# Kernel optimization log

Hardware: AMD Instinct MI355X
Metric: run time of the kernel (lower is better)

Reference implementation:

```python
import jax, jax.numpy as jnp
import numpy as np
import math

LOG2 = math.log(2)
B, N, H, E, M = 128, 2048, 300, 20, 200
IN = 3 * H + 3 * E  # 960: [mem, query, mem*query, 3 feature embs]
NEG = -10000.0


def _bucket(x):
    # floor(log2(x)) + 3 for x > 4, identity for x <= 4, clamped to [0, 9]
    xf = x.astype(jnp.float32)
    logspace = jnp.floor(jnp.log(jnp.maximum(xf, 1.0)) / LOG2).astype(jnp.int32) + 3
    return jnp.clip(jnp.where(x <= 4, x, logspace), 0, 9)


def setup_inputs() -> dict:
    key = jax.random.key(0)
    ks = jax.random.split(key, 12)
    return {
        "query_vector": jax.random.normal(ks[0], (B, H), jnp.float32),
        "ment_score": jax.random.normal(ks[1], (B,), jnp.float32),
        "mem_vectors": jax.random.normal(ks[2], (B, N, H), jnp.float32),
        "ent_counter": jax.random.randint(ks[3], (B, N), 0, 20, jnp.int32),
        "distances": jax.random.randint(ks[4], (B, N), 0, 5000, jnp.int32),
        "last_action_idx": jax.random.randint(ks[5], (B,), 0, 5, jnp.int32),
        "cell_idx": jax.random.randint(ks[6], (B,), 0, N, jnp.int32),
        "W1": jax.random.normal(ks[7], (IN, M), jnp.float32) / np.sqrt(IN),
        "b1": jnp.zeros((M,), jnp.float32),
        "W2": jax.random.normal(ks[8], (M, 1), jnp.float32) / np.sqrt(M),
        "b2": jnp.zeros((1,), jnp.float32),
        "dist_table": jax.random.normal(ks[9], (10, E), jnp.float32),
        "count_table": jax.random.normal(ks[10], (10, E), jnp.float32),
        "action_table": jax.random.normal(ks[11], (5, E), jnp.float32),
    }


def reference(query_vector, ment_score, mem_vectors, ent_counter, distances,
              last_action_idx, cell_idx, W1, b1, W2, b2,
              dist_table, count_table, action_table):
    # ---- feature embeddings (get_feature_embs, litbank: dist+counter+last_action) ----
    dist_emb = dist_table[_bucket(distances)]            # [B, N, E]
    cnt_emb = count_table[_bucket(ent_counter)]          # [B, N, E]
    act_emb = jnp.broadcast_to(action_table[last_action_idx][:, None, :], (B, N, E))
    feature_embs = jnp.concatenate([dist_emb, cnt_emb, act_emb], axis=-1)  # [B, N, 3E]

    # ---- get_coref_new_scores ----
    q = jnp.broadcast_to(query_vector[:, None, :], (B, N, H))
    pair_vec = jnp.concatenate([mem_vectors, q, mem_vectors * q, feature_embs], axis=-1)  # [B, N, IN]
    hdn = jax.nn.relu(jnp.einsum('bni,im->bnm', pair_vec, W1) + b1)
    pair_score = (jnp.einsum('bnm,mo->bno', hdn, W2) + b2)[..., 0]  # [B, N]
    coref_score = pair_score + ment_score[:, None]

    mask = (ent_counter > 0).astype(jnp.float32)                            # [B, N]
    full_mask = jnp.concatenate([mask, jnp.ones((B, 1), jnp.float32)], axis=1)
    full_score = jnp.concatenate([coref_score, jnp.zeros((B, 1), jnp.float32)], axis=1)
    coref_new_scores = full_score * full_mask + (1.0 - full_mask) * NEG     # [B, N+1]

    # ---- coref_update (entity_rep='max' default branch: running average + masked scatter) ----
    brange = jnp.arange(B)
    cnt_sel = ent_counter[brange, cell_idx].astype(jnp.float32)             # [B]
    mem_sel = mem_vectors[brange, cell_idx]                                 # [B, H]
    avg_vec = (mem_sel * cnt_sel[:, None] + query_vector) / (cnt_sel[:, None] + 1.0)
    onehot = (jnp.arange(N)[None, :] == cell_idx[:, None]).astype(jnp.float32)[:, :, None]  # [B, N, 1]
    new_mem = mem_vectors * (1.0 - onehot) + onehot * avg_vec[:, None, :]

    return coref_new_scores, new_mem
```

## Files before the change

### kernel.cpp

```cpp
#include <hip/hip_runtime.h>
#include <math.h>

#define BB 128
#define NN 2048
#define HH 300
#define EE 20
#define MM 200
#define NEGV (-10000.0f)
#define SCORES_OFF (BB * (NN + 1))

#define NCOL 208
#define KSTEPS 10
#define ROWSH 72
#define KIMG (NCOL * ROWSH)
#define BIMG_SHORTS ((size_t)BB * KSTEPS * KIMG)
#define FWS_FLOATS (BB * MM + 10 * MM + 10 * MM + BB * HH)

typedef short bf16x8 __attribute__((ext_vector_type(8)));
typedef float f32x4 __attribute__((ext_vector_type(4)));

__device__ __forceinline__ int bucketf(int x) {
  if (x <= 4) return x < 0 ? 0 : x;
  float l = floorf(logf((float)x) / 0.69314718055994530942f);
  int bi = (int)l + 3;
  return bi > 9 ? 9 : bi;
}

__device__ __forceinline__ short f2bf(float f) {
  union { float f; unsigned u; } v; v.f = f;
  unsigned r = (v.u + 0x7FFFu + ((v.u >> 16) & 1u)) >> 16;
  return (short)r;
}
__device__ __forceinline__ float bf2f(short s) {
  union { unsigned u; float f; } v; v.u = ((unsigned)(unsigned short)s) << 16;
  return v.f;
}

__global__ void k_small(const float* __restrict__ W1, const float* __restrict__ b1,
                        const float* __restrict__ q, const float* __restrict__ mem,
                        const float* __restrict__ dtab, const float* __restrict__ ctab,
                        const float* __restrict__ atab, const int* __restrict__ lact,
                        const int* __restrict__ entc, const int* __restrict__ cell,
                        float* __restrict__ distW, float* __restrict__ cntW,
                        float* __restrict__ bias, float* __restrict__ avg,
                        float* __restrict__ out) {
  const int blk = blockIdx.x;
  const int tid = threadIdx.x;
  if (blk < 13) {
    int idx = blk * 320 + tid;
    if (idx >= 2 * 10 * MM) return;
    int t = idx / (10 * MM);
    int r = idx % (10 * MM);
    int d = r / MM;
    int m = r % MM;
    const float* tab = (t == 0) ? dtab : ctab;
    int wrow0 = (t == 0) ? (3 * HH) : (3 * HH + EE);
    float s = 0.f;
#pragma unroll
    for (int e = 0; e < EE; e++) s += tab[d * EE + e] * W1[(wrow0 + e) * MM + m];
    ((t == 0) ? distW : cntW)[d * MM + m] = s;
  } else if (blk < 93) {
    int idx = (blk - 13) * 320 + tid;
    if (idx >= BB * MM) return;
    int b = idx / MM;
    int m = idx % MM;
    float s = b1[m];
    for (int h = 0; h < HH; h++) s += q[b * HH + h] * W1[(HH + h) * MM + m];
    int la = lact[b];
#pragma unroll
    for (int e = 0; e < EE; e++)
      s += atab[la * EE + e] * W1[(3 * HH + 2 * EE + e) * MM + m];
    bias[idx] = s;
  } else {
    int b = blk - 93;
    int ci = cell[b];
    if (tid < HH) {
      float c = (float)entc[b * NN + ci];
      float m = mem[((size_t)b * NN + ci) * HH + tid];
      avg[b * HH + tid] = (m * c + q[b * HH + tid]) / (c + 1.f);
    } else if (tid == HH) {
      out[b * (NN + 1) + NN] = 0.f;
    }
  }
}

__global__ void k_prep(const float* __restrict__ W1, const float* __restrict__ q,
                       short* __restrict__ Bimg) {
  int idx = blockIdx.x * blockDim.x + threadIdx.x;
  if (idx >= BB * KSTEPS * NCOL) return;
  int col = idx % NCOL;
  int bks = idx / NCOL;
  int ks = bks % KSTEPS;
  int b = bks / KSTEPS;
  int k0 = ks * 32;
  const float* qb = q + b * HH;

  __align__(16) short buf[ROWSH];
#pragma unroll
  for (int g = 0; g < 4; g++) {
#pragma unroll
    for (int i = 0; i < 8; i++) {
      int k = k0 + 8 * g + i;
      float val = 0.f;
      if (k < HH && col < MM) {
        val = fmaf(qb[k], W1[(size_t)(2 * HH + k) * MM + col],
                   W1[(size_t)k * MM + col]);
      }
      short h = f2bf(val);
      buf[g * 8 + i] = h;
      buf[32 + g * 8 + i] = f2bf(val - bf2f(h));
    }
  }
#pragma unroll
  for (int i = 64; i < 72; i++) buf[i] = 0;

  float4* dst = (float4*)(Bimg + (size_t)idx * ROWSH);
  const float4* src = (const float4*)buf;
#pragma unroll
  for (int i = 0; i < 9; i++) dst[i] = src[i];
}

__device__ __forceinline__ void epilogue(
    const f32x4* acc, int b, int n0, int w, int lr, int g,
    const float* __restrict__ bias, const float* __restrict__ distW,
    const float* __restrict__ cntW, const float* __restrict__ W2,
    const float* __restrict__ b2, const float* __restrict__ ment,
    const int* __restrict__ entc, const int* __restrict__ dist,
    float* __restrict__ out) {
  const float addc = b2[0] + ment[b];
  const float* bi = bias + b * MM;
  float s[4];
#pragma unroll
  for (int r = 0; r < 4; r++) {
    int nr = n0 + w * 16 + 4 * g + r;
    int db = bucketf(dist[b * NN + nr]);
    int cb = bucketf(entc[b * NN + nr]);
    const float* dW = distW + db * MM;
    const float* cW = cntW + cb * MM;
    float acc_s = 0.f;
#pragma unroll
    for (int f = 0; f < 13; f++) {
      if (f < 12 || lr < 8) {
        int m = f * 16 + lr;
        float h = acc[f][r] + bi[m] + dW[m] + cW[m];
        acc_s += fmaxf(h, 0.f) * W2[m];
      }
    }
    s[r] = acc_s;
  }
#pragma unroll
  for (int off = 1; off < 16; off <<= 1) {
#pragma unroll
    for (int r = 0; r < 4; r++) s[r] += __shfl_xor(s[r], off);
  }
  if (lr == 0) {
#pragma unroll
    for (int r = 0; r < 4; r++) {
      int nr = n0 + w * 16 + 4 * g + r;
      int mk = entc[b * NN + nr] > 0;
      out[b * (NN + 1) + nr] = mk ? (s[r] + addc) : NEGV;
    }
  }
}

__device__ __forceinline__ void load_a(
    const float* rowp, float* orow, const float* avgp, bool subst, int kb,
    bf16x8* ahi, bf16x8* alo) {
  float va[8];
  if (kb + 7 < HH) {
    float4 x0 = *(const float4*)(rowp + kb);
    float4 x1 = *(const float4*)(rowp + kb + 4);
    va[0] = x0.x; va[1] = x0.y; va[2] = x0.z; va[3] = x0.w;
    va[4] = x1.x; va[5] = x1.y; va[6] = x1.z; va[7] = x1.w;
    float4 o0 = x0, o1 = x1;
    if (subst) {
      o0 = *(const float4*)(avgp + kb);
      o1 = *(const float4*)(avgp + kb + 4);
    }
    *(float4*)(orow + kb) = o0;
    *(float4*)(orow + kb + 4) = o1;
  } else {
#pragma unroll
    for (int i = 0; i < 8; i++) {
      int k = kb + i;
      bool ok = (k < HH);
      va[i] = ok ? rowp[k] : 0.f;
      if (ok) orow[k] = subst ? avgp[k] : va[i];
    }
  }
#pragma unroll
  for (int i = 0; i < 8; i++) {
    short h = f2bf(va[i]);
    (*ahi)[i] = h;
    (*alo)[i] = f2bf(va[i] - bf2f(h));
  }
}

__global__ __launch_bounds__(256, 3) void k_main(
    const float* __restrict__ mem, const short* __restrict__ Bimg,
    const float* __restrict__ bias, const float* __restrict__ distW,
    const float* __restrict__ cntW, const float* __restrict__ W2,
    const float* __restrict__ b2, const float* __restrict__ ment,
    const int* __restrict__ entc, const int* __restrict__ dist,
    const int* __restrict__ cell, const float* __restrict__ avg,
    float* __restrict__ out) {
  __shared__ __align__(16) short btS[KIMG];

  const int tid = threadIdx.x;
  const int bid = blockIdx.x;
  const int b = (bid & 7) * 16 + (bid >> 8);
  const int n0 = ((bid >> 3) & 31) * 64;

  const int w = tid >> 6;
  const int l = tid & 63;
  const int lr = l & 15;
  const int g = l >> 4;

  const int ci = cell[b];
  const int n = n0 + w * 16 + lr;
  const float* rowp = mem + ((size_t)b * NN + n) * HH;
  float* orow = out + SCORES_OFF + ((size_t)b * NN + n) * HH;
  const float* avgp = avg + b * HH;
  const bool subst = (n == ci);

  f32x4 acc[13];
#pragma unroll
  for (int f = 0; f < 13; f++) acc[f] = (f32x4){0.f, 0.f, 0.f, 0.f};

  for (int ks = 0; ks < KSTEPS; ks++) {
    bf16x8 ahi, alo;
    load_a(rowp, orow, avgp, subst, ks * 32 + 8 * g, &ahi, &alo);

    __syncthreads();
    {
      const float4* bsrc = (const float4*)(Bimg + (size_t)(b * KSTEPS + ks) * KIMG);
      float4* bdst = (float4*)btS;
      for (int i = tid; i < KIMG / 8; i += 256) bdst[i] = bsrc[i];
    }
    __syncthreads();

#pragma unroll
    for (int f = 0; f < 13; f++) {
      const short* bp = &btS[(f * 16 + lr) * ROWSH + g * 8];
      bf16x8 bhi = *(const bf16x8*)bp;
      bf16x8 blo = *(const bf16x8*)(bp + 32);
      acc[f] = __builtin_amdgcn_mfma_f32_16x16x32_bf16(ahi, bhi, acc[f], 0, 0, 0);
      acc[f] = __builtin_amdgcn_mfma_f32_16x16x32_bf16(alo, bhi, acc[f], 0, 0, 0);
      acc[f] = __builtin_amdgcn_mfma_f32_16x16x32_bf16(ahi, blo, acc[f], 0, 0, 0);
    }
  }

  epilogue(acc, b, n0, w, lr, g, bias, distW, cntW, W2, b2, ment, entc, dist, out);
}

__global__ __launch_bounds__(256, 3) void k_main_fb(
    const float* __restrict__ mem, const float* __restrict__ W1,
    const float* __restrict__ q, const float* __restrict__ bias,
    const float* __restrict__ distW, const float* __restrict__ cntW,
    const float* __restrict__ W2, const float* __restrict__ b2,
    const float* __restrict__ ment, const int* __restrict__ entc,
    const int* __restrict__ dist, const int* __restrict__ cell,
    const float* __restrict__ avg, float* __restrict__ out) {
  __shared__ __align__(16) short btS[KIMG];

  const int tid = threadIdx.x;
  const int b = blockIdx.y;
  const int n0 = blockIdx.x * 64;
  const int w = tid >> 6;
  const int l = tid & 63;
  const int lr = l & 15;
  const int g = l >> 4;

  const int ci = cell[b];
  const int n = n0 + w * 16 + lr;
  const float* rowp = mem + ((size_t)b * NN + n) * HH;
  float* orow = out + SCORES_OFF + ((size_t)b * NN + n) * HH;
  const float* avgp = avg + b * HH;
  const bool subst = (n == ci);
  const float* qb = q + b * HH;

  f32x4 acc[13];
#pragma unroll
  for (int f = 0; f < 13; f++) acc[f] = (f32x4){0.f, 0.f, 0.f, 0.f};

  for (int ks = 0; ks < KSTEPS; ks++) {
    const int k0 = ks * 32;
    bf16x8 ahi, alo;
    load_a(rowp, orow, avgp, subst, k0 + 8 * g, &ahi, &alo);

    __syncthreads();
    for (int it = 0; it < 4; it++) {
      int idx = tid + it * 256;
      if (idx < 832) {
        int col = idx % NCOL;
        int gg = idx / NCOL;
        int kbb = k0 + 8 * gg;
        bf16x8 h8, l8;
#pragma unroll
        for (int i = 0; i < 8; i++) {
          int k = kbb + i;
          float val = 0.f;
          if (k < HH && col < MM) {
            val = fmaf(qb[k], W1[(size_t)(2 * HH + k) * MM + col],
                       W1[(size_t)k * MM + col]);
          }
          short h = f2bf(val);
          h8[i] = h;
          l8[i] = f2bf(val - bf2f(h));
        }
        short* dst = &btS[col * ROWSH + gg * 8];
        *(bf16x8*)dst = h8;
        *(bf16x8*)(dst + 32) = l8;
      }
    }
    __syncthreads();

#pragma unroll
    for (int f = 0; f < 13; f++) {
      const short* bp = &btS[(f * 16 + lr) * ROWSH + g * 8];
      bf16x8 bhi = *(const bf16x8*)bp;
      bf16x8 blo = *(const bf16x8*)(bp + 32);
      acc[f] = __builtin_amdgcn_mfma_f32_16x16x32_bf16(ahi, bhi, acc[f], 0, 0, 0);
      acc[f] = __builtin_amdgcn_mfma_f32_16x16x32_bf16(alo, bhi, acc[f], 0, 0, 0);
      acc[f] = __builtin_amdgcn_mfma_f32_16x16x32_bf16(ahi, blo, acc[f], 0, 0, 0);
    }
  }

  epilogue(acc, b, n0, w, lr, g, bias, distW, cntW, W2, b2, ment, entc, dist, out);
}

extern "C" void kernel_launch(void* const* d_in, const int* in_sizes, int n_in,
                              void* d_out, int out_size, void* d_ws, size_t ws_size,
                              hipStream_t stream) {
  const float* q    = (const float*)d_in[0];
  const float* ment = (const float*)d_in[1];
  const float* mem  = (const float*)d_in[2];
  const int* entc   = (const int*)d_in[3];
  const int* dist   = (const int*)d_in[4];
  const int* lact   = (const int*)d_in[5];
  const int* cell   = (const int*)d_in[6];
  const float* W1   = (const float*)d_in[7];
  const float* b1   = (const float*)d_in[8];
  const float* W2   = (const float*)d_in[9];
  const float* b2   = (const float*)d_in[10];
  const float* dtab = (const float*)d_in[11];
  const float* ctab = (const float*)d_in[12];
  const float* atab = (const float*)d_in[13];
  float* out = (float*)d_out;

  const size_t need_fast = BIMG_SHORTS * sizeof(short) + FWS_FLOATS * sizeof(float);
  const bool fast = (ws_size >= need_fast);

  short* Bimg = (short*)d_ws;
  float* fws  = fast ? (float*)(Bimg + BIMG_SHORTS) : (float*)d_ws;
  float* bias  = fws;
  float* distW = bias + BB * MM;
  float* cntW  = distW + 10 * MM;
  float* avg   = cntW + 10 * MM;

  k_small<<<221, 320, 0, stream>>>(W1, b1, q, mem, dtab, ctab, atab, lact,
                                   entc, cell, distW, cntW, bias, avg, out);
  if (fast) {
    k_prep<<<(BB * KSTEPS * NCOL) / 256, 256, 0, stream>>>(W1, q, Bimg);
    k_main<<<4096, 256, 0, stream>>>(mem, Bimg, bias, distW, cntW, W2, b2,
                                     ment, entc, dist, cell, avg, out);
  } else {
    k_main_fb<<<dim3(NN / 64, BB), 256, 0, stream>>>(
        mem, W1, q, bias, distW, cntW, W2, b2, ment, entc, dist, cell, avg, out);
  }
}
```

Before: 775.0 us.

## Double-buffer B tiles via global_load_lds and prefetch A rows in main GEMM

Measured after the change: 708.3 us. -8.6%, faster.

```diff
diff --git a/kernel.cpp b/kernel.cpp
--- a/kernel.cpp
+++ b/kernel.cpp
@@ -13,8 +13,8 @@
 #define KSTEPS 10
 #define ROWSH 72
 #define KIMG (NCOL * ROWSH)
+#define CH16 (KIMG / 8)
 #define BIMG_SHORTS ((size_t)BB * KSTEPS * KIMG)
-#define FWS_FLOATS (BB * MM + 10 * MM + 10 * MM + BB * HH)
 
 typedef short bf16x8 __attribute__((ext_vector_type(8)));
 typedef float f32x4 __attribute__((ext_vector_type(4)));
@@ -36,14 +36,20 @@
   return v.f;
 }
 
-__global__ void k_small(const float* __restrict__ W1, const float* __restrict__ b1,
+__device__ __forceinline__ void gload16(const void* g, void* l) {
+  __builtin_amdgcn_global_load_lds(
+      (const __attribute__((address_space(1))) void*)g,
+      (__attribute__((address_space(3))) void*)l, 16, 0, 0);
+}
+
+__global__ void k_prep2(const float* __restrict__ W1, const float* __restrict__ b1,
                         const float* __restrict__ q, const float* __restrict__ mem,
                         const float* __restrict__ dtab, const float* __restrict__ ctab,
                         const float* __restrict__ atab, const int* __restrict__ lact,
                         const int* __restrict__ entc, const int* __restrict__ cell,
                         float* __restrict__ distW, float* __restrict__ cntW,
                         float* __restrict__ bias, float* __restrict__ avg,
-                        float* __restrict__ out) {
+                        short* __restrict__ Bimg, float* __restrict__ out) {
   const int blk = blockIdx.x;
   const int tid = threadIdx.x;
   if (blk < 13) {
@@ -71,7 +77,7 @@
     for (int e = 0; e < EE; e++)
       s += atab[la * EE + e] * W1[(3 * HH + 2 * EE + e) * MM + m];
     bias[idx] = s;
-  } else {
+  } else if (blk < 221) {
     int b = blk - 93;
     int ci = cell[b];
     if (tid < HH) {
@@ -81,43 +87,81 @@
     } else if (tid == HH) {
       out[b * (NN + 1) + NN] = 0.f;
     }
-  }
-}
-
-__global__ void k_prep(const float* __restrict__ W1, const float* __restrict__ q,
-                       short* __restrict__ Bimg) {
-  int idx = blockIdx.x * blockDim.x + threadIdx.x;
-  if (idx >= BB * KSTEPS * NCOL) return;
-  int col = idx % NCOL;
-  int bks = idx / NCOL;
-  int ks = bks % KSTEPS;
-  int b = bks / KSTEPS;
-  int k0 = ks * 32;
-  const float* qb = q + b * HH;
-
-  __align__(16) short buf[ROWSH];
-#pragma unroll
-  for (int g = 0; g < 4; g++) {
+  } else {
+    int idx = (blk - 221) * 320 + tid;
+    int col = idx % NCOL;
+    int bks = idx / NCOL;
+    int ks = bks % KSTEPS;
+    int b = bks / KSTEPS;
+    int k0 = ks * 32;
+    const float* qb = q + b * HH;
+    short* dst = Bimg + (size_t)idx * ROWSH;
+#pragma unroll
+    for (int g = 0; g < 4; g++) {
+      bf16x8 h8, l8;
+#pragma unroll
+      for (int i = 0; i < 8; i++) {
+        int k = k0 + 8 * g + i;
+        float val = 0.f;
+        if (k < HH && col < MM) {
+          val = fmaf(qb[k], W1[(size_t)(2 * HH + k) * MM + col],
+                     W1[(size_t)k * MM + col]);
+        }
+        short h = f2bf(val);
+        h8[i] = h;
+        l8[i] = f2bf(val - bf2f(h));
+      }
+      *(bf16x8*)(dst + g * 8) = h8;
+      *(bf16x8*)(dst + 32 + g * 8) = l8;
+    }
+    *(bf16x8*)(dst + 64) = (bf16x8){0, 0, 0, 0, 0, 0, 0, 0};
+  }
+}
+
+__device__ __forceinline__ void issueA(const float* rowp, int kb, float* va) {
+  if (kb + 7 < HH) {
+    float4 x0 = *(const float4*)(rowp + kb);
+    float4 x1 = *(const float4*)(rowp + kb + 4);
+    va[0] = x0.x; va[1] = x0.y; va[2] = x0.z; va[3] = x0.w;
+    va[4] = x1.x; va[5] = x1.y; va[6] = x1.z; va[7] = x1.w;
+  } else {
 #pragma unroll
     for (int i = 0; i < 8; i++) {
-      int k = k0 + 8 * g + i;
-      float val = 0.f;
-      if (k < HH && col < MM) {
-        val = fmaf(qb[k], W1[(size_t)(2 * HH + k) * MM + col],
-                   W1[(size_t)k * MM + col]);
-      }
-      short h = f2bf(val);
-      buf[g * 8 + i] = h;
-      buf[32 + g * 8 + i] = f2bf(val - bf2f(h));
-    }
-  }
-#pragma unroll
-  for (int i = 64; i < 72; i++) buf[i] = 0;
-
-  float4* dst = (float4*)(Bimg + (size_t)idx * ROWSH);
-  const float4* src = (const float4*)buf;
-#pragma unroll
-  for (int i = 0; i < 9; i++) dst[i] = src[i];
+      int k = kb + i;
+      va[i] = (k < HH) ? rowp[k] : 0.f;
+    }
+  }
+}
+
+__device__ __forceinline__ void storeA(const float* va, int kb, float* orow,
+                                       const float* avgp, bool subst) {
+  if (kb + 7 < HH) {
+    float4 o0, o1;
+    if (subst) {
+      o0 = *(const float4*)(avgp + kb);
+      o1 = *(const float4*)(avgp + kb + 4);
+    } else {
+      o0 = make_float4(va[0], va[1], va[2], va[3]);
+      o1 = make_float4(va[4], va[5], va[6], va[7]);
+    }
+    *(float4*)(orow + kb) = o0;
+    *(float4*)(orow + kb + 4) = o1;
+  } else {
+#pragma unroll
+    for (int i = 0; i < 8; i++) {
+      int k = kb + i;
+      if (k < HH) orow[k] = subst ? avgp[k] : va[i];
+    }
+  }
+}
+
+__device__ __forceinline__ void cvtA(const float* va, bf16x8* ahi, bf16x8* alo) {
+#pragma unroll
+  for (int i = 0; i < 8; i++) {
+    short h = f2bf(va[i]);
+    (*ahi)[i] = h;
+    (*alo)[i] = f2bf(va[i] - bf2f(h));
+  }
 }
 
 __device__ __forceinline__ void epilogue(
@@ -163,40 +207,7 @@
   }
 }
 
-__device__ __forceinline__ void load_a(
-    const float* rowp, float* orow, const float* avgp, bool subst, int kb,
-    bf16x8* ahi, bf16x8* alo) {
-  float va[8];
-  if (kb + 7 < HH) {
-    float4 x0 = *(const float4*)(rowp + kb);
-    float4 x1 = *(const float4*)(rowp + kb + 4);
-    va[0] = x0.x; va[1] = x0.y; va[2] = x0.z; va[3] = x0.w;
-    va[4] = x1.x; va[5] = x1.y; va[6] = x1.z; va[7] = x1.w;
-    float4 o0 = x0, o1 = x1;
-    if (subst) {
-      o0 = *(const float4*)(avgp + kb);
-      o1 = *(const float4*)(avgp + kb + 4);
-    }
-    *(float4*)(orow + kb) = o0;
-    *(float4*)(orow + kb + 4) = o1;
-  } else {
-#pragma unroll
-    for (int i = 0; i < 8; i++) {
-      int k = kb + i;
-      bool ok = (k < HH);
-      va[i] = ok ? rowp[k] : 0.f;
-      if (ok) orow[k] = subst ? avgp[k] : va[i];
-    }
-  }
-#pragma unroll
-  for (int i = 0; i < 8; i++) {
-    short h = f2bf(va[i]);
-    (*ahi)[i] = h;
-    (*alo)[i] = f2bf(va[i] - bf2f(h));
-  }
-}
-
-__global__ __launch_bounds__(256, 3) void k_main(
+__global__ __launch_bounds__(512, 4) void k_main(
     const float* __restrict__ mem, const short* __restrict__ Bimg,
     const float* __restrict__ bias, const float* __restrict__ distW,
     const float* __restrict__ cntW, const float* __restrict__ W2,
@@ -204,12 +215,12 @@
     const int* __restrict__ entc, const int* __restrict__ dist,
     const int* __restrict__ cell, const float* __restrict__ avg,
     float* __restrict__ out) {
-  __shared__ __align__(16) short btS[KIMG];
+  __shared__ __align__(16) short btS[2][KIMG];
 
   const int tid = threadIdx.x;
   const int bid = blockIdx.x;
-  const int b = (bid & 7) * 16 + (bid >> 8);
-  const int n0 = ((bid >> 3) & 31) * 64;
+  const int b = (bid & 7) * 16 + (bid >> 7);
+  const int n0 = ((bid >> 3) & 15) * 128;
 
   const int w = tid >> 6;
   const int l = tid & 63;
@@ -222,107 +233,53 @@
   float* orow = out + SCORES_OFF + ((size_t)b * NN + n) * HH;
   const float* avgp = avg + b * HH;
   const bool subst = (n == ci);
+  const short* bsrc = Bimg + (size_t)b * KSTEPS * KIMG;
 
   f32x4 acc[13];
 #pragma unroll
   for (int f = 0; f < 13; f++) acc[f] = (f32x4){0.f, 0.f, 0.f, 0.f};
 
+  float va[8];
+  issueA(rowp, 8 * g, va);
+#pragma unroll
+  for (int it = 0; it < 4; it++) {
+    int i = tid + it * 512;
+    if (i < CH16) gload16(bsrc + (size_t)i * 8, &btS[0][i * 8]);
+  }
+  bf16x8 ahi, alo;
+  cvtA(va, &ahi, &alo);
+  __syncthreads();
+
   for (int ks = 0; ks < KSTEPS; ks++) {
-    bf16x8 ahi, alo;
-    load_a(rowp, orow, avgp, subst, ks * 32 + 8 * g, &ahi, &alo);
-
-    __syncthreads();
-    {
-      const float4* bsrc = (const float4*)(Bimg + (size_t)(b * KSTEPS + ks) * KIMG);
-      float4* bdst = (float4*)btS;
-      for (int i = tid; i < KIMG / 8; i += 256) bdst[i] = bsrc[i];
-    }
-    __syncthreads();
+    const int cur = ks & 1;
+    const int kb_cur = ks * 32 + 8 * g;
+    float vn[8];
+    if (ks < KSTEPS - 1) {
+      const short* bs = bsrc + (size_t)(ks + 1) * KIMG;
+#pragma unroll
+      for (int it = 0; it < 4; it++) {
+        int i = tid + it * 512;
+        if (i < CH16) gload16(bs + (size_t)i * 8, &btS[cur ^ 1][i * 8]);
+      }
+      issueA(rowp, kb_cur + 32, vn);
+    }
+    storeA(va, kb_cur, orow, avgp, subst);
 
 #pragma unroll
     for (int f = 0; f < 13; f++) {
-      const short* bp = &btS[(f * 16 + lr) * ROWSH + g * 8];
+      const short* bp = &btS[cur][(f * 16 + lr) * ROWSH + g * 8];
       bf16x8 bhi = *(const bf16x8*)bp;
       bf16x8 blo = *(const bf16x8*)(bp + 32);
       acc[f] = __builtin_amdgcn_mfma_f32_16x16x32_bf16(ahi, bhi, acc[f], 0, 0, 0);
       acc[f] = __builtin_amdgcn_mfma_f32_16x16x32_bf16(alo, bhi, acc[f], 0, 0, 0);
       acc[f] = __builtin_amdgcn_mfma_f32_16x16x32_bf16(ahi, blo, acc[f], 0, 0, 0);
     }
-  }
-
-  epilogue(acc, b, n0, w, lr, g, bias, distW, cntW, W2, b2, ment, entc, dist, out);
-}
-
-__global__ __launch_bounds__(256, 3) void k_main_fb(
-    const float* __restrict__ mem, const float* __restrict__ W1,
-    const float* __restrict__ q, const float* __restrict__ bias,
-    const float* __restrict__ distW, const float* __restrict__ cntW,
-    const float* __restrict__ W2, const float* __restrict__ b2,
-    const float* __restrict__ ment, const int* __restrict__ entc,
-    const int* __restrict__ dist, const int* __restrict__ cell,
-    const float* __restrict__ avg, float* __restrict__ out) {
-  __shared__ __align__(16) short btS[KIMG];
-
-  const int tid = threadIdx.x;
-  const int b = blockIdx.y;
-  const int n0 = blockIdx.x * 64;
-  const int w = tid >> 6;
-  const int l = tid & 63;
-  const int lr = l & 15;
-  const int g = l >> 4;
-
-  const int ci = cell[b];
-  const int n = n0 + w * 16 + lr;
-  const float* rowp = mem + ((size_t)b * NN + n) * HH;
-  float* orow = out + SCORES_OFF + ((size_t)b * NN + n) * HH;
-  const float* avgp = avg + b * HH;
-  const bool subst = (n == ci);
-  const float* qb = q + b * HH;
-
-  f32x4 acc[13];
-#pragma unroll
-  for (int f = 0; f < 13; f++) acc[f] = (f32x4){0.f, 0.f, 0.f, 0.f};
-
-  for (int ks = 0; ks < KSTEPS; ks++) {
-    const int k0 = ks * 32;
-    bf16x8 ahi, alo;
-    load_a(rowp, orow, avgp, subst, k0 + 8 * g, &ahi, &alo);
-
-    __syncthreads();
-    for (int it = 0; it < 4; it++) {
-      int idx = tid + it * 256;
-      if (idx < 832) {
-        int col = idx % NCOL;
-        int gg = idx / NCOL;
-        int kbb = k0 + 8 * gg;
-        bf16x8 h8, l8;
-#pragma unroll
-        for (int i = 0; i < 8; i++) {
-          int k = kbb + i;
-          float val = 0.f;
-          if (k < HH && col < MM) {
-            val = fmaf(qb[k], W1[(size_t)(2 * HH + k) * MM + col],
-                       W1[(size_t)k * MM + col]);
-          }
-          short h = f2bf(val);
-          h8[i] = h;
-          l8[i] = f2bf(val - bf2f(h));
-        }
-        short* dst = &btS[col * ROWSH + gg * 8];
-        *(bf16x8*)dst = h8;
-        *(bf16x8*)(dst + 32) = l8;
-      }
-    }
-    __syncthreads();
-
-#pragma unroll
-    for (int f = 0; f < 13; f++) {
-      const short* bp = &btS[(f * 16 + lr) * ROWSH + g * 8];
-      bf16x8 bhi = *(const bf16x8*)bp;
-      bf16x8 blo = *(const bf16x8*)(bp + 32);
-      acc[f] = __builtin_amdgcn_mfma_f32_16x16x32_bf16(ahi, bhi, acc[f], 0, 0, 0);
-      acc[f] = __builtin_amdgcn_mfma_f32_16x16x32_bf16(alo, bhi, acc[f], 0, 0, 0);
-      acc[f] = __builtin_amdgcn_mfma_f32_16x16x32_bf16(ahi, blo, acc[f], 0, 0, 0);
+
+    if (ks < KSTEPS - 1) {
+#pragma unroll
+      for (int i = 0; i < 8; i++) va[i] = vn[i];
+      cvtA(va, &ahi, &alo);
+      __syncthreads();
     }
   }
 
@@ -348,24 +305,15 @@
   const float* atab = (const float*)d_in[13];
   float* out = (float*)d_out;
 
-  const size_t need_fast = BIMG_SHORTS * sizeof(short) + FWS_FLOATS * sizeof(float);
-  const bool fast = (ws_size >= need_fast);
-
-  short* Bimg = (short*)d_ws;
-  float* fws  = fast ? (float*)(Bimg + BIMG_SHORTS) : (float*)d_ws;
+  short* Bimg  = (short*)d_ws;
+  float* fws   = (float*)(Bimg + BIMG_SHORTS);
   float* bias  = fws;
   float* distW = bias + BB * MM;
   float* cntW  = distW + 10 * MM;
   float* avg   = cntW + 10 * MM;
 
-  k_small<<<221, 320, 0, stream>>>(W1, b1, q, mem, dtab, ctab, atab, lact,
-                                   entc, cell, distW, cntW, bias, avg, out);
-  if (fast) {
-    k_prep<<<(BB * KSTEPS * NCOL) / 256, 256, 0, stream>>>(W1, q, Bimg);
-    k_main<<<4096, 256, 0, stream>>>(mem, Bimg, bias, distW, cntW, W2, b2,
-                                     ment, entc, dist, cell, avg, out);
-  } else {
-    k_main_fb<<<dim3(NN / 64, BB), 256, 0, stream>>>(
-        mem, W1, q, bias, distW, cntW, W2, b2, ment, entc, dist, cell, avg, out);
-  }
-}
+  k_prep2<<<1053, 320, 0, stream>>>(W1, b1, q, mem, dtab, ctab, atab, lact,
+                                    entc, cell, distW, cntW, bias, avg, Bimg, out);
+  k_main<<<2048, 512, 0, stream>>>(mem, Bimg, bias, distW, cntW, W2, b2, ment,
+                                   entc, dist, cell, avg, out);
+}
```
